# Performance work log

Measured on AMD Instinct MI355X. Metric: run time of the kernel, lower is better.

Reference implementation:

```python
import jax, jax.numpy as jnp
import numpy as np

B = 256          # graphs per batch
N_PER_G = 64     # nodes per graph
E_PER_G = 1024   # edges per graph
FN, FE, FG = 128, 128, 64
NA, HA, SO = 8, 256, 128


def _w(key, shape, scale=0.05):
    return jax.random.normal(key, shape, dtype=jnp.float32) * scale


def setup_inputs() -> dict:
    key = jax.random.key(0)
    ks = jax.random.split(key, 24)
    TN, TE = B * N_PER_G, B * E_PER_G
    inp = {
        'nodes': jax.random.normal(ks[0], (TN, FN), dtype=jnp.float32),
        'edges': jax.random.normal(ks[1], (TE, FE), dtype=jnp.float32),
        'globals_': jax.random.normal(ks[2], (B, FG), dtype=jnp.float32),
        'node_graph': jnp.repeat(jnp.arange(B, dtype=jnp.int32), N_PER_G),
        'edge_graph': jnp.repeat(jnp.arange(B, dtype=jnp.int32), E_PER_G),
        'a': jax.random.normal(ks[3], (B, NA), dtype=jnp.float32),
        # edge1: EdgeLinear(256, edge_features=FE)
        'We1': _w(ks[4], (FE, 256)), 'be1': jnp.zeros((256,), jnp.float32),
        # node1: NodeLinear(256, node_features=FN)
        'Wn1': _w(ks[5], (FN, 256)), 'bn1': jnp.zeros((256,), jnp.float32),
        # edge2: EdgeLinear(128, edge_features=256, global_features=FG)
        'We2_e': _w(ks[6], (256, 128)), 'We2_g': _w(ks[7], (FG, 128)), 'be2': jnp.zeros((128,), jnp.float32),
        # node2: NodeLinear(128, node_features=256, global_features=FG)
        'Wn2_n': _w(ks[8], (256, 128)), 'Wn2_g': _w(ks[9], (FG, 128)), 'bn2': jnp.zeros((128,), jnp.float32),
        # global: GlobalLinear(SO, node_features=128, edge_features=128, global_features=FG, aggregation='avg')
        'Wg_n': _w(ks[10], (128, SO)), 'Wg_e': _w(ks[11], (128, SO)), 'Wg_g': _w(ks[12], (FG, SO)), 'bg': jnp.zeros((SO,), jnp.float32),
        # action MLP
        'Wh': _w(ks[13], (SO + NA, HA)), 'bh': jnp.zeros((HA,), jnp.float32),
        'Wo': _w(ks[14], (HA, 1)), 'bo': jnp.zeros((1,), jnp.float32),
    }
    return inp


def _seg_mean(x, seg, num_segments):
    s = jax.ops.segment_sum(x, seg, num_segments=num_segments)
    c = jax.ops.segment_sum(jnp.ones((x.shape[0],), x.dtype), seg, num_segments=num_segments)
    return s / jnp.maximum(c, 1.0)[:, None]


def reference(nodes, edges, globals_, node_graph, edge_graph, a,
              We1, be1, Wn1, bn1, We2_e, We2_g, be2, Wn2_n, Wn2_g, bn2,
              Wg_n, Wg_e, Wg_g, bg, Wh, bh, Wo, bo):
    nb = globals_.shape[0]
    # edge1 + relu
    e = jax.nn.relu(edges @ We1 + be1)                                  # [TE,256]
    # node1 + relu
    n = jax.nn.relu(nodes @ Wn1 + bn1)                                  # [TN,256]
    # edge2 (edge feats + global broadcast to edges) + relu
    e = jax.nn.relu(e @ We2_e + globals_[edge_graph] @ We2_g + be2)     # [TE,128]
    # node2 (node feats + global broadcast to nodes) + relu
    n = jax.nn.relu(n @ Wn2_n + globals_[node_graph] @ Wn2_g + bn2)     # [TN,128]
    # global: avg-aggregate nodes and edges per graph + global linear
    n_avg = _seg_mean(n, node_graph, nb)                                # [B,128]
    e_avg = _seg_mean(e, edge_graph, nb)                                # [B,128]
    state_value = n_avg @ Wg_n + e_avg @ Wg_e + globals_ @ Wg_g + bg    # [B,SO]
    # action MLP
    sa = jnp.concatenate((state_value, a), axis=1)                      # [B,SO+NA]
    h = jax.nn.relu(sa @ Wh + bh)                                       # [B,HA]
    return h @ Wo + bo                                                  # [B,1]
```

## Files before the change

### kernel.cpp

```cpp
#include <hip/hip_runtime.h>

typedef unsigned short u16;
typedef __attribute__((ext_vector_type(8))) short s8v;
typedef __attribute__((ext_vector_type(4))) float f4v;

__device__ __forceinline__ float bf2f(u16 u) {
    union { unsigned int i; float f; } v;
    v.i = ((unsigned int)u) << 16;
    return v.f;
}
__device__ __forceinline__ u16 f2bf(float f) {
    union { float f; unsigned int i; } v;
    v.f = f;
    unsigned int x = v.i;
    x += 0x7FFFu + ((x >> 16) & 1u);
    return (u16)(x >> 16);
}
__device__ __forceinline__ float ldx(const void* p, long long i, int isf) {
    return isf ? ((const float*)p)[i] : bf2f(((const u16*)p)[i]);
}

__device__ __forceinline__ int probe_isf(const void* W) {
    const u16* p = (const u16*)W;
    int cnt = 0;
#pragma unroll
    for (int i = 0; i < 32; ++i) {
        u16 u = p[2 * i];
        int e = (u >> 7) & 0xFF;
        cnt += ((e == 0) || (e >= 96 && e <= 140)) ? 1 : 0;
    }
    return (cnt < 16) ? 1 : 0;
}

__global__ void diag_kernel(const void* W, int* flag) {
    __shared__ int cnt;
    int t = threadIdx.x;
    if (t == 0) cnt = 0;
    __syncthreads();
    u16 u = ((const u16*)W)[2 * t];
    int e = (u >> 7) & 0xFF;
    int plausible = (e == 0) || (e >= 96 && e <= 140);
    atomicAdd(&cnt, plausible);
    __syncthreads();
    if (t == 0) *flag = (cnt < 128) ? 1 : 0;
}

__global__ void magic_kernel(void* out, float code) {
    ((u16*)out)[threadIdx.x] = f2bf(code);
}

__global__ void prep2_kernel(const void* We2_g, const void* Wn2_g,
                             const void* globals_,
                             const void* We1, const void* Wn1,
                             const void* We2_e, const void* Wn2_n,
                             float* sums_zero, float* G2e, float* G2n,
                             u16* W1e_p, u16* W2e_p, u16* W1n_p, u16* W2n_p)
{
    int isf = probe_isf(We1);
    int t = blockIdx.x * 256 + threadIdx.x;
    if (t < 65536) { sums_zero[t] = 0.f; return; }
    if (t < 131072) {
        int i = t - 65536;
        int which = i >> 15;
        int idx = i & 32767;
        int g = idx >> 7, c = idx & 127;
        const void* Wg = which ? Wn2_g : We2_g;
        float s = 0.f;
#pragma unroll 8
        for (int k = 0; k < 64; ++k)
            s += ldx(globals_, g * 64 + k, isf) * ldx(Wg, k * 128 + c, isf);
        if (which) G2n[idx] = s; else G2e[idx] = s;
        return;
    }
    int p = t - 131072;
    int which = p >> 12;
    int idx = p & 4095;
    int f = idx >> 6, lj = idx & 63;
    const void* W; u16* dst; int kb, nt, N;
    if (which == 0)      { W = We1;   dst = W1e_p; kb = f >> 4; nt = f & 15; N = 256; }
    else if (which == 1) { W = Wn1;   dst = W1n_p; kb = f >> 4; nt = f & 15; N = 256; }
    else if (which == 2) { W = We2_e; dst = W2e_p; kb = f >> 3; nt = f & 7;  N = 128; }
    else                 { W = Wn2_n; dst = W2n_p; kb = f >> 3; nt = f & 7;  N = 128; }
    int k0 = kb * 32 + 8 * (lj >> 4);
    int n  = nt * 16 + (lj & 15);
    s8v v;
#pragma unroll
    for (int j = 0; j < 8; ++j)
        v[j] = (short)f2bf(ldx(W, (long long)(k0 + j) * N + n, isf));
    *(s8v*)&dst[f * 512 + lj * 8] = v;
}

__global__ __launch_bounds__(256, 4) void QNetwork_89103391522965_kernel(
    const void* edges, const void* nodes,
    const void* be1, const void* bn1, const void* be2, const void* bn2,
    const u16* W1e, const u16* W2e, const u16* W1n, const u16* W2n,
    const float* G2e, const float* G2n,
    float* e_sum, float* n_sum, const void* probeW)
{
    __shared__ u16 E1[64 * 256];
    __shared__ float accb[128];

    const int isf  = probe_isf(probeW);
    const int tid  = threadIdx.x;
    const int lane = tid & 63;
    const int w    = tid >> 6;
    const int l15  = lane & 15;
    const int lg   = lane >> 4;

    const int bid = blockIdx.x;
    const bool isn = bid >= 4096;
    const void* X   = isn ? nodes : edges;
    const void* b1  = isn ? bn1 : be1;
    const void* b2  = isn ? bn2 : be2;
    const u16* W1p  = isn ? W1n : W1e;
    const u16* W2p  = isn ? W2n : W2e;
    const float* gt = isn ? G2n : G2e;
    float* sum      = isn ? n_sum : e_sum;
    const int m0    = (isn ? (bid - 4096) : bid) * 64;
    const int g     = isn ? (bid - 4096) : (bid >> 4);

    if (tid < 128) accb[tid] = 0.f;

    f4v acc1[4][4];
#pragma unroll
    for (int nj = 0; nj < 4; ++nj) {
        float bv = ldx(b1, 64 * w + 16 * nj + l15, isf);
#pragma unroll
        for (int mi = 0; mi < 4; ++mi) {
            f4v t = {bv, bv, bv, bv};
            acc1[mi][nj] = t;
        }
    }

#pragma unroll
    for (int kb = 0; kb < 4; ++kb) {
        s8v a[4];
        const int k0 = kb * 32 + 8 * lg;
        if (!isf) {
#pragma unroll
            for (int mi = 0; mi < 4; ++mi)
                a[mi] = *(const s8v*)((const u16*)X +
                         (long long)(m0 + 16 * mi + l15) * 128 + k0);
        } else {
#pragma unroll
            for (int mi = 0; mi < 4; ++mi) {
                const float* xf = (const float*)X +
                         (long long)(m0 + 16 * mi + l15) * 128 + k0;
                s8v v;
#pragma unroll
                for (int j = 0; j < 8; ++j) v[j] = (short)f2bf(xf[j]);
                a[mi] = v;
            }
        }
#pragma unroll
        for (int nj = 0; nj < 4; ++nj) {
            s8v b = *(const s8v*)&W1p[(kb * 16 + 4 * w + nj) * 512 + lane * 8];
#pragma unroll
            for (int mi = 0; mi < 4; ++mi)
                acc1[mi][nj] = __builtin_amdgcn_mfma_f32_16x16x32_bf16(
                    a[mi], b, acc1[mi][nj], 0, 0, 0);
        }
    }

#pragma unroll
    for (int mi = 0; mi < 4; ++mi) {
#pragma unroll
        for (int nj = 0; nj < 4; ++nj) {
            int col = 64 * w + 16 * nj + l15;
#pragma unroll
            for (int r = 0; r < 4; ++r) {
                int row = 16 * mi + 4 * lg + r;
                int sw  = ((row ^ (row >> 1)) & 7) << 3;
                E1[(row * 256 + col) ^ sw] = f2bf(fmaxf(acc1[mi][nj][r], 0.f));
            }
        }
    }
    __syncthreads();

    f4v acc2[2][4];
#pragma unroll
    for (int mp = 0; mp < 2; ++mp)
#pragma unroll
        for (int nj = 0; nj < 4; ++nj) {
            f4v z = {0.f, 0.f, 0.f, 0.f};
            acc2[mp][nj] = z;
        }
    const int mb16  = (w >> 1) * 32;
    const int nbase = (w & 1) * 4;

#pragma unroll
    for (int kb = 0; kb < 8; ++kb) {
        s8v a2[2];
#pragma unroll
        for (int mp = 0; mp < 2; ++mp) {
            int row = mb16 + mp * 16 + l15;
            int sw  = ((row ^ (row >> 1)) & 7) << 3;
            a2[mp] = *(const s8v*)&E1[(row * 256 + kb * 32 + lg * 8) ^ sw];
        }
#pragma unroll
        for (int nj = 0; nj < 4; ++nj) {
            s8v b = *(const s8v*)&W2p[(kb * 8 + nbase + nj) * 512 + lane * 8];
#pragma unroll
            for (int mp = 0; mp < 2; ++mp)
                acc2[mp][nj] = __builtin_amdgcn_mfma_f32_16x16x32_bf16(
                    a2[mp], b, acc2[mp][nj], 0, 0, 0);
        }
    }

#pragma unroll
    for (int nj = 0; nj < 4; ++nj) {
        int c2 = (nbase + nj) * 16 + l15;
        float add = gt[g * 128 + c2] + ldx(b2, c2, isf);
        float s = 0.f;
#pragma unroll
        for (int mp = 0; mp < 2; ++mp)
#pragma unroll
            for (int r = 0; r < 4; ++r)
                s += fmaxf(acc2[mp][nj][r] + add, 0.f);
        s += __shfl_xor(s, 16);
        s += __shfl_xor(s, 32);
        if (lg == 0)
            atomicAdd(&accb[c2], s);
    }
    __syncthreads();
    if (tid < 128)
        atomicAdd(&sum[g * 128 + tid], accb[tid]);
}

__global__ void prep_kernel(const void* We2_g, const void* Wn2_g,
                            const void* globals_, const int* flag,
                            float* sums_zero, float* G2e, float* G2n)
{
    int isf = *flag;
    int t = blockIdx.x * 256 + threadIdx.x;
    if (t < 65536) {
        sums_zero[t] = 0.f;
    } else {
        int i = t - 65536;
        int which = i >> 15;
        int idx = i & 32767;
        int g = idx >> 7, c = idx & 127;
        const void* Wg = which ? Wn2_g : We2_g;
        float s = 0.f;
        for (int k = 0; k < 64; ++k)
            s += ldx(globals_, g * 64 + k, isf) * ldx(Wg, k * 128 + c, isf);
        if (which) G2n[idx] = s; else G2e[idx] = s;
    }
}

__global__ void QNetwork_89103391522965_valu(
    const void* X, const void* W1, const void* b1,
    const void* W2, const void* b2, const float* gterm,
    const int* flag, float* sum_out, int rows_per_graph)
{
    __shared__ u16 Xs[64 * 132];
    __shared__ u16 E1[64 * 260];
    __shared__ float accb[128];

    int isf = *flag;
    int tid = threadIdx.x;
    int m0 = blockIdx.x * 64;
    int g = m0 / rows_per_graph;

    if (tid < 128) accb[tid] = 0.f;

    for (int i = 0; i < 32; ++i) {
        int f = tid + i * 256;
        int row = f >> 7, col = f & 127;
        Xs[row * 132 + col] =
            f2bf(ldx(X, (long long)(m0 + row) * 128 + col, isf));
    }
    __syncthreads();

    {
        int c = tid;
        float binit = ldx(b1, c, isf);
        for (int rc = 0; rc < 4; ++rc) {
            float acc[16];
#pragma unroll
            for (int i = 0; i < 16; ++i) acc[i] = binit;
            for (int k = 0; k < 128; k += 2) {
                float w0 = ldx(W1, k * 256 + c, isf);
                float w1 = ldx(W1, (k + 1) * 256 + c, isf);
#pragma unroll
                for (int i = 0; i < 16; ++i) {
                    unsigned int xx =
                        *(const unsigned int*)&Xs[(rc * 16 + i) * 132 + k];
                    acc[i] += bf2f((u16)(xx & 0xFFFFu)) * w0;
                    acc[i] += bf2f((u16)(xx >> 16)) * w1;
                }
            }
#pragma unroll
            for (int i = 0; i < 16; ++i)
                E1[(rc * 16 + i) * 260 + c] = f2bf(fmaxf(acc[i], 0.f));
        }
    }
    __syncthreads();

    {
        int c2 = tid & 127;
        int rh = tid >> 7;
        float add = gterm[g * 128 + c2] + ldx(b2, c2, isf);
        float rowsum = 0.f;
        for (int rc = 0; rc < 2; ++rc) {
            int r0 = rh * 32 + rc * 16;
            float acc[16];
#pragma unroll
            for (int i = 0; i < 16; ++i) acc[i] = 0.f;
            for (int k = 0; k < 256; k += 2) {
                float w0 = ldx(W2, k * 128 + c2, isf);
                float w1 = ldx(W2, (k + 1) * 128 + c2, isf);
#pragma unroll
                for (int i = 0; i < 16; ++i) {
                    unsigned int xx =
                        *(const unsigned int*)&E1[(r0 + i) * 260 + k];
                    acc[i] += bf2f((u16)(xx & 0xFFFFu)) * w0;
                    acc[i] += bf2f((u16)(xx >> 16)) * w1;
                }
            }
#pragma unroll
            for (int i = 0; i < 16; ++i)
                rowsum += fmaxf(acc[i] + add, 0.f);
        }
        atomicAdd(&accb[c2], rowsum);
    }
    __syncthreads();
    if (tid < 128) atomicAdd(&sum_out[g * 128 + tid], accb[tid]);
}

__global__ void final_kernel(
    const float* e_sum, const float* n_sum,
    const void* globals_, const void* a_in,
    const void* Wg_n, const void* Wg_e, const void* Wg_g, const void* bg,
    const void* Wh, const void* bh, const void* Wo, const void* bo,
    const void* probeW, void* out)
{
    __shared__ float navg[128], eavg[128], gv[64], sa[136];
    __shared__ float red[4];
    int isf = probe_isf(probeW);
    int g = blockIdx.x, t = threadIdx.x;

    if (t < 128) {
        navg[t] = n_sum[g * 128 + t] * (1.f / 64.f);
        eavg[t] = e_sum[g * 128 + t] * (1.f / 1024.f);
    } else if (t < 192) {
        gv[t - 128] = ldx(globals_, g * 64 + (t - 128), isf);
    }
    __syncthreads();

    if (t < 128) {
        float s = ldx(bg, t, isf);
#pragma unroll 8
        for (int k = 0; k < 128; ++k) s += navg[k] * ldx(Wg_n, k * 128 + t, isf);
#pragma unroll 8
        for (int k = 0; k < 128; ++k) s += eavg[k] * ldx(Wg_e, k * 128 + t, isf);
#pragma unroll 8
        for (int k = 0; k < 64;  ++k) s += gv[k]   * ldx(Wg_g, k * 128 + t, isf);
        sa[t] = s;
    } else if (t < 136) {
        sa[t] = ldx(a_in, g * 8 + (t - 128), isf);
    }
    __syncthreads();

    float s = ldx(bh, t, isf);
#pragma unroll 8
    for (int k = 0; k < 136; ++k) s += sa[k] * ldx(Wh, k * 256 + t, isf);
    float hv = fmaxf(s, 0.f) * ldx(Wo, t, isf);
#pragma unroll
    for (int off = 32; off; off >>= 1) hv += __shfl_down(hv, off);
    if ((t & 63) == 0) red[t >> 6] = hv;
    __syncthreads();
    if (t == 0) {
        float val = red[0] + red[1] + red[2] + red[3] + ldx(bo, 0, isf);
        if (isf) ((float*)out)[g] = val;
        else     ((u16*)out)[g]   = f2bf(val);
    }
}

extern "C" void kernel_launch(void* const* d_in, const int* in_sizes, int n_in,
                              void* d_out, int out_size, void* d_ws, size_t ws_size,
                              hipStream_t stream) {
    static const int EXPECT[24] = {
        2097152, 33554432, 16384, 16384, 262144, 2048,
        32768, 256, 32768, 256,
        32768, 8192, 128, 32768, 8192, 128,
        16384, 16384, 8192, 128,
        34816, 256, 256, 1
    };
    float code = 0.f;
    if (n_in != 24) code = 3000.f + n_in;
    else {
        for (int i = 0; i < 24; ++i)
            if (in_sizes[i] != EXPECT[i]) { code = 1000.f + i; break; }
    }
    if (ws_size < 524292 && code == 0.f) code = 4000.f;
    if (code != 0.f) {
        magic_kernel<<<1, 256, 0, stream>>>(d_out, code);
        return;
    }

    const void* nodes    = d_in[0];
    const void* edges    = d_in[1];
    const void* globals_ = d_in[2];
    const void* a_in  = d_in[5];
    const void* We1   = d_in[6];
    const void* be1   = d_in[7];
    const void* Wn1   = d_in[8];
    const void* bn1   = d_in[9];
    const void* We2_e = d_in[10];
    const void* We2_g = d_in[11];
    const void* be2   = d_in[12];
    const void* Wn2_n = d_in[13];
    const void* Wn2_g = d_in[14];
    const void* bn2   = d_in[15];
    const void* Wg_n  = d_in[16];
    const void* Wg_e  = d_in[17];
    const void* Wg_g  = d_in[18];
    const void* bg    = d_in[19];
    const void* Wh    = d_in[20];
    const void* bh    = d_in[21];
    const void* Wo    = d_in[22];
    const void* bo    = d_in[23];

    char* ws = (char*)d_ws;
    float* e_sum = (float*)(ws + 0);
    float* n_sum = (float*)(ws + 131072);
    float* G2e   = (float*)(ws + 262144);
    float* G2n   = (float*)(ws + 393216);

    if (ws_size >= 786436) {
        u16* W1e_p = (u16*)(ws + 524288);
        u16* W2e_p = (u16*)(ws + 589824);
        u16* W1n_p = (u16*)(ws + 655360);
        u16* W2n_p = (u16*)(ws + 720896);

        prep2_kernel<<<576, 256, 0, stream>>>(We2_g, Wn2_g, globals_,
                                              We1, Wn1, We2_e, Wn2_n,
                                              e_sum, G2e, G2n,
                                              W1e_p, W2e_p, W1n_p, W2n_p);
        QNetwork_89103391522965_kernel<<<4352, 256, 0, stream>>>(
            edges, nodes, be1, bn1, be2, bn2,
            W1e_p, W2e_p, W1n_p, W2n_p, G2e, G2n,
            e_sum, n_sum, We1);
        final_kernel<<<256, 256, 0, stream>>>(e_sum, n_sum, globals_, a_in,
                                              Wg_n, Wg_e, Wg_g, bg, Wh, bh, Wo, bo,
                                              We1, d_out);
    } else {
        int* flag = (int*)(ws + 524288);
        diag_kernel<<<1, 256, 0, stream>>>(We1, flag);
        prep_kernel<<<512, 256, 0, stream>>>(We2_g, Wn2_g, globals_, flag,
                                             e_sum, G2e, G2n);
        QNetwork_89103391522965_valu<<<4096, 256, 0, stream>>>(
            edges, We1, be1, We2_e, be2, G2e, flag, e_sum, 1024);
        QNetwork_89103391522965_valu<<<256, 256, 0, stream>>>(
            nodes, Wn1, bn1, Wn2_n, bn2, G2n, flag, n_sum, 64);
        final_kernel<<<256, 256, 0, stream>>>(e_sum, n_sum, globals_, a_in,
                                              Wg_n, Wg_e, Wg_g, bg, Wh, bh, Wo, bo,
                                              We1, d_out);
    }
}
```

Before: 373.8 us.

## Halve per-block row tile to 32 and cache dtype probe flag in workspace

The fused two-layer MLP kernel now handles 32 rows per block instead of 64. This halves the shared-memory staging buffer and the accumulator registers, doubles the grid, and raises the launch-bounds occupancy hint from 4 to 6 blocks per CU. The per-block dtype probe (a shared atomic vote over weight bits) is replaced by a flag written once in the prep kernel and read from the workspace by the main and final kernels. The trade-off is more blocks and more global atomics into the per-graph sums, and weight fragments are reloaded more often relative to the rows processed.

New measurement: 428.7 us. +14.7%, slower.

```diff
diff --git a/kernel.cpp b/kernel.cpp
--- a/kernel.cpp
+++ b/kernel.cpp
@@ -54,10 +54,12 @@
                              const void* We1, const void* Wn1,
                              const void* We2_e, const void* Wn2_n,
                              float* sums_zero, float* G2e, float* G2n,
-                             u16* W1e_p, u16* W2e_p, u16* W1n_p, u16* W2n_p)
+                             u16* W1e_p, u16* W2e_p, u16* W1n_p, u16* W2n_p,
+                             int* flagp)
 {
     int isf = probe_isf(We1);
     int t = blockIdx.x * 256 + threadIdx.x;
+    if (t == 0) *flagp = isf;
     if (t < 65536) { sums_zero[t] = 0.f; return; }
     if (t < 131072) {
         int i = t - 65536;
@@ -90,17 +92,17 @@
     *(s8v*)&dst[f * 512 + lj * 8] = v;
 }
 
-__global__ __launch_bounds__(256, 4) void QNetwork_89103391522965_kernel(
+__global__ __launch_bounds__(256, 6) void QNetwork_89103391522965_kernel(
     const void* edges, const void* nodes,
     const void* be1, const void* bn1, const void* be2, const void* bn2,
     const u16* W1e, const u16* W2e, const u16* W1n, const u16* W2n,
     const float* G2e, const float* G2n,
-    float* e_sum, float* n_sum, const void* probeW)
+    float* e_sum, float* n_sum, const int* flagp)
 {
-    __shared__ u16 E1[64 * 256];
+    __shared__ u16 E1[32 * 256];
     __shared__ float accb[128];
 
-    const int isf  = probe_isf(probeW);
+    const int isf  = *flagp;
     const int tid  = threadIdx.x;
     const int lane = tid & 63;
     const int w    = tid >> 6;
@@ -108,7 +110,8 @@
     const int lg   = lane >> 4;
 
     const int bid = blockIdx.x;
-    const bool isn = bid >= 4096;
+    const bool isn = bid >= 8192;
+    const int rb = isn ? (bid - 8192) : bid;
     const void* X   = isn ? nodes : edges;
     const void* b1  = isn ? bn1 : be1;
     const void* b2  = isn ? bn2 : be2;
@@ -116,107 +119,93 @@
     const u16* W2p  = isn ? W2n : W2e;
     const float* gt = isn ? G2n : G2e;
     float* sum      = isn ? n_sum : e_sum;
-    const int m0    = (isn ? (bid - 4096) : bid) * 64;
-    const int g     = isn ? (bid - 4096) : (bid >> 4);
+    const int m0    = rb * 32;
+    const int g     = isn ? (rb >> 1) : (rb >> 5);
 
     if (tid < 128) accb[tid] = 0.f;
 
-    f4v acc1[4][4];
+    const int nbase = (w & 1) * 4;
+    const int mi2   = (w >> 1);
+
+    float binit[4];
+#pragma unroll
+    for (int nj = 0; nj < 4; ++nj)
+        binit[nj] = ldx(b1, 64 * w + 16 * nj + l15, isf);
+    float add[4];
 #pragma unroll
     for (int nj = 0; nj < 4; ++nj) {
-        float bv = ldx(b1, 64 * w + 16 * nj + l15, isf);
-#pragma unroll
-        for (int mi = 0; mi < 4; ++mi) {
-            f4v t = {bv, bv, bv, bv};
-            acc1[mi][nj] = t;
-        }
-    }
-
-#pragma unroll
-    for (int kb = 0; kb < 4; ++kb) {
-        s8v a[4];
-        const int k0 = kb * 32 + 8 * lg;
-        if (!isf) {
-#pragma unroll
-            for (int mi = 0; mi < 4; ++mi)
-                a[mi] = *(const s8v*)((const u16*)X +
-                         (long long)(m0 + 16 * mi + l15) * 128 + k0);
-        } else {
-#pragma unroll
-            for (int mi = 0; mi < 4; ++mi) {
-                const float* xf = (const float*)X +
-                         (long long)(m0 + 16 * mi + l15) * 128 + k0;
+        int c2 = (nbase + nj) * 16 + l15;
+        add[nj] = gt[g * 128 + c2] + ldx(b2, c2, isf);
+    }
+
+#pragma unroll
+    for (int mh = 0; mh < 2; ++mh) {
+        f4v acc1[4];
+#pragma unroll
+        for (int nj = 0; nj < 4; ++nj) {
+            f4v tv = {binit[nj], binit[nj], binit[nj], binit[nj]};
+            acc1[nj] = tv;
+        }
+#pragma unroll
+        for (int kb = 0; kb < 4; ++kb) {
+            const int k0 = kb * 32 + 8 * lg;
+            const int row = m0 + 16 * mh + l15;
+            s8v a;
+            if (!isf) {
+                a = *(const s8v*)((const u16*)X + (long long)row * 128 + k0);
+            } else {
+                const float* xf = (const float*)X + (long long)row * 128 + k0;
                 s8v v;
 #pragma unroll
                 for (int j = 0; j < 8; ++j) v[j] = (short)f2bf(xf[j]);
-                a[mi] = v;
+                a = v;
             }
-        }
-#pragma unroll
-        for (int nj = 0; nj < 4; ++nj) {
-            s8v b = *(const s8v*)&W1p[(kb * 16 + 4 * w + nj) * 512 + lane * 8];
-#pragma unroll
-            for (int mi = 0; mi < 4; ++mi)
-                acc1[mi][nj] = __builtin_amdgcn_mfma_f32_16x16x32_bf16(
-                    a[mi], b, acc1[mi][nj], 0, 0, 0);
-        }
-    }
-
-#pragma unroll
-    for (int mi = 0; mi < 4; ++mi) {
+#pragma unroll
+            for (int nj = 0; nj < 4; ++nj) {
+                s8v b = *(const s8v*)&W1p[(kb * 16 + 4 * w + nj) * 512 + lane * 8];
+                acc1[nj] = __builtin_amdgcn_mfma_f32_16x16x32_bf16(
+                    a, b, acc1[nj], 0, 0, 0);
+            }
+        }
 #pragma unroll
         for (int nj = 0; nj < 4; ++nj) {
             int col = 64 * w + 16 * nj + l15;
 #pragma unroll
             for (int r = 0; r < 4; ++r) {
-                int row = 16 * mi + 4 * lg + r;
+                int row = 16 * mh + 4 * lg + r;
                 int sw  = ((row ^ (row >> 1)) & 7) << 3;
-                E1[(row * 256 + col) ^ sw] = f2bf(fmaxf(acc1[mi][nj][r], 0.f));
+                E1[(row * 256 + col) ^ sw] = f2bf(fmaxf(acc1[nj][r], 0.f));
             }
         }
     }
     __syncthreads();
 
-    f4v acc2[2][4];
-#pragma unroll
-    for (int mp = 0; mp < 2; ++mp)
-#pragma unroll
-        for (int nj = 0; nj < 4; ++nj) {
-            f4v z = {0.f, 0.f, 0.f, 0.f};
-            acc2[mp][nj] = z;
-        }
-    const int mb16  = (w >> 1) * 32;
-    const int nbase = (w & 1) * 4;
-
+    f4v acc2[4];
+#pragma unroll
+    for (int nj = 0; nj < 4; ++nj) {
+        f4v z = {0.f, 0.f, 0.f, 0.f};
+        acc2[nj] = z;
+    }
 #pragma unroll
     for (int kb = 0; kb < 8; ++kb) {
-        s8v a2[2];
-#pragma unroll
-        for (int mp = 0; mp < 2; ++mp) {
-            int row = mb16 + mp * 16 + l15;
-            int sw  = ((row ^ (row >> 1)) & 7) << 3;
-            a2[mp] = *(const s8v*)&E1[(row * 256 + kb * 32 + lg * 8) ^ sw];
-        }
+        int row = 16 * mi2 + l15;
+        int sw  = ((row ^ (row >> 1)) & 7) << 3;
+        s8v a2 = *(const s8v*)&E1[(row * 256 + kb * 32 + lg * 8) ^ sw];
 #pragma unroll
         for (int nj = 0; nj < 4; ++nj) {
             s8v b = *(const s8v*)&W2p[(kb * 8 + nbase + nj) * 512 + lane * 8];
-#pragma unroll
-            for (int mp = 0; mp < 2; ++mp)
-                acc2[mp][nj] = __builtin_amdgcn_mfma_f32_16x16x32_bf16(
-                    a2[mp], b, acc2[mp][nj], 0, 0, 0);
+            acc2[nj] = __builtin_amdgcn_mfma_f32_16x16x32_bf16(
+                a2, b, acc2[nj], 0, 0, 0);
         }
     }
 
 #pragma unroll
     for (int nj = 0; nj < 4; ++nj) {
         int c2 = (nbase + nj) * 16 + l15;
-        float add = gt[g * 128 + c2] + ldx(b2, c2, isf);
         float s = 0.f;
 #pragma unroll
-        for (int mp = 0; mp < 2; ++mp)
-#pragma unroll
-            for (int r = 0; r < 4; ++r)
-                s += fmaxf(acc2[mp][nj][r] + add, 0.f);
+        for (int r = 0; r < 4; ++r)
+            s += fmaxf(acc2[nj][r] + add[nj], 0.f);
         s += __shfl_xor(s, 16);
         s += __shfl_xor(s, 32);
         if (lg == 0)
@@ -333,11 +322,11 @@
     const void* globals_, const void* a_in,
     const void* Wg_n, const void* Wg_e, const void* Wg_g, const void* bg,
     const void* Wh, const void* bh, const void* Wo, const void* bo,
-    const void* probeW, void* out)
+    const int* flagp, void* out)
 {
     __shared__ float navg[128], eavg[128], gv[64], sa[136];
     __shared__ float red[4];
-    int isf = probe_isf(probeW);
+    int isf = *flagp;
     int g = blockIdx.x, t = threadIdx.x;
 
     if (t < 128) {
@@ -428,23 +417,25 @@
     float* G2e   = (float*)(ws + 262144);
     float* G2n   = (float*)(ws + 393216);
 
-    if (ws_size >= 786436) {
+    if (ws_size >= 786440) {
         u16* W1e_p = (u16*)(ws + 524288);
         u16* W2e_p = (u16*)(ws + 589824);
         u16* W1n_p = (u16*)(ws + 655360);
         u16* W2n_p = (u16*)(ws + 720896);
+        int* flagp = (int*)(ws + 786432);
 
         prep2_kernel<<<576, 256, 0, stream>>>(We2_g, Wn2_g, globals_,
                                               We1, Wn1, We2_e, Wn2_n,
                                               e_sum, G2e, G2n,
-                                              W1e_p, W2e_p, W1n_p, W2n_p);
-        QNetwork_89103391522965_kernel<<<4352, 256, 0, stream>>>(
+                                              W1e_p, W2e_p, W1n_p, W2n_p,
+                                              flagp);
+        QNetwork_89103391522965_kernel<<<8704, 256, 0, stream>>>(
             edges, nodes, be1, bn1, be2, bn2,
             W1e_p, W2e_p, W1n_p, W2n_p, G2e, G2n,
-            e_sum, n_sum, We1);
+            e_sum, n_sum, flagp);
         final_kernel<<<256, 256, 0, stream>>>(e_sum, n_sum, globals_, a_in,
                                               Wg_n, Wg_e, Wg_g, bg, Wh, bh, Wo, bo,
-                                              We1, d_out);
+                                              flagp, d_out);
     } else {
         int* flag = (int*)(ws + 524288);
         diag_kernel<<<1, 256, 0, stream>>>(We1, flag);
@@ -456,6 +447,6 @@
             nodes, Wn1, bn1, Wn2_n, bn2, G2n, flag, n_sum, 64);
         final_kernel<<<256, 256, 0, stream>>>(e_sum, n_sum, globals_, a_in,
                                               Wg_n, Wg_e, Wg_g, bg, Wh, bh, Wo, bo,
-                                              We1, d_out);
-    }
-}
+                                              flag, d_out);
+    }
+}
```

## Process four 64-row tiles per block and cache dtype probe flag

Applied to the files above, without the earlier changes.

The fused MLP kernel now has each block loop over four 64-row tiles, so the grid shrinks from 4352 to 1088 blocks. Edge partial sums are kept in registers across tiles and hit global memory with one atomic per graph. Node tiles write their per-graph sums directly instead of using atomics. The per-kernel dtype probe is replaced by a flag computed once in prep2 and read from workspace. The cost is fewer blocks in flight and serialized tiles inside each block, with no overlap between a tile's loads and the previous tile's compute.

Result: slower. 780.7 us (+108.8%).

```diff
diff --git a/kernel.cpp b/kernel.cpp
--- a/kernel.cpp
+++ b/kernel.cpp
@@ -54,10 +54,12 @@
                              const void* We1, const void* Wn1,
                              const void* We2_e, const void* Wn2_n,
                              float* sums_zero, float* G2e, float* G2n,
-                             u16* W1e_p, u16* W2e_p, u16* W1n_p, u16* W2n_p)
+                             u16* W1e_p, u16* W2e_p, u16* W1n_p, u16* W2n_p,
+                             int* flagp)
 {
     int isf = probe_isf(We1);
     int t = blockIdx.x * 256 + threadIdx.x;
+    if (t == 0) *flagp = isf;
     if (t < 65536) { sums_zero[t] = 0.f; return; }
     if (t < 131072) {
         int i = t - 65536;
@@ -95,12 +97,12 @@
     const void* be1, const void* bn1, const void* be2, const void* bn2,
     const u16* W1e, const u16* W2e, const u16* W1n, const u16* W2n,
     const float* G2e, const float* G2n,
-    float* e_sum, float* n_sum, const void* probeW)
+    float* e_sum, float* n_sum, const int* flagp)
 {
     __shared__ u16 E1[64 * 256];
     __shared__ float accb[128];
 
-    const int isf  = probe_isf(probeW);
+    const int isf  = *flagp;
     const int tid  = threadIdx.x;
     const int lane = tid & 63;
     const int w    = tid >> 6;
@@ -108,123 +110,155 @@
     const int lg   = lane >> 4;
 
     const int bid = blockIdx.x;
-    const bool isn = bid >= 4096;
+    const bool isn = bid >= 1024;
+    const int rb = isn ? (bid - 1024) : bid;
     const void* X   = isn ? nodes : edges;
     const void* b1  = isn ? bn1 : be1;
     const void* b2  = isn ? bn2 : be2;
     const u16* W1p  = isn ? W1n : W1e;
     const u16* W2p  = isn ? W2n : W2e;
     const float* gt = isn ? G2n : G2e;
-    float* sum      = isn ? n_sum : e_sum;
-    const int m0    = (isn ? (bid - 4096) : bid) * 64;
-    const int g     = isn ? (bid - 4096) : (bid >> 4);
+    const int base  = rb * 256;
+    const int ge    = bid >> 2;
 
     if (tid < 128) accb[tid] = 0.f;
 
-    f4v acc1[4][4];
-#pragma unroll
-    for (int nj = 0; nj < 4; ++nj) {
-        float bv = ldx(b1, 64 * w + 16 * nj + l15, isf);
-#pragma unroll
-        for (int mi = 0; mi < 4; ++mi) {
-            f4v t = {bv, bv, bv, bv};
-            acc1[mi][nj] = t;
-        }
-    }
-
-#pragma unroll
-    for (int kb = 0; kb < 4; ++kb) {
-        s8v a[4];
-        const int k0 = kb * 32 + 8 * lg;
-        if (!isf) {
-#pragma unroll
-            for (int mi = 0; mi < 4; ++mi)
-                a[mi] = *(const s8v*)((const u16*)X +
-                         (long long)(m0 + 16 * mi + l15) * 128 + k0);
-        } else {
-#pragma unroll
-            for (int mi = 0; mi < 4; ++mi) {
-                const float* xf = (const float*)X +
-                         (long long)(m0 + 16 * mi + l15) * 128 + k0;
-                s8v v;
-#pragma unroll
-                for (int j = 0; j < 8; ++j) v[j] = (short)f2bf(xf[j]);
-                a[mi] = v;
-            }
-        }
-#pragma unroll
-        for (int nj = 0; nj < 4; ++nj) {
-            s8v b = *(const s8v*)&W1p[(kb * 16 + 4 * w + nj) * 512 + lane * 8];
-#pragma unroll
-            for (int mi = 0; mi < 4; ++mi)
-                acc1[mi][nj] = __builtin_amdgcn_mfma_f32_16x16x32_bf16(
-                    a[mi], b, acc1[mi][nj], 0, 0, 0);
-        }
-    }
-
-#pragma unroll
-    for (int mi = 0; mi < 4; ++mi) {
-#pragma unroll
-        for (int nj = 0; nj < 4; ++nj) {
-            int col = 64 * w + 16 * nj + l15;
-#pragma unroll
-            for (int r = 0; r < 4; ++r) {
-                int row = 16 * mi + 4 * lg + r;
-                int sw  = ((row ^ (row >> 1)) & 7) << 3;
-                E1[(row * 256 + col) ^ sw] = f2bf(fmaxf(acc1[mi][nj][r], 0.f));
-            }
-        }
-    }
-    __syncthreads();
-
-    f4v acc2[2][4];
-#pragma unroll
-    for (int mp = 0; mp < 2; ++mp)
-#pragma unroll
-        for (int nj = 0; nj < 4; ++nj) {
-            f4v z = {0.f, 0.f, 0.f, 0.f};
-            acc2[mp][nj] = z;
-        }
     const int mb16  = (w >> 1) * 32;
     const int nbase = (w & 1) * 4;
 
-#pragma unroll
-    for (int kb = 0; kb < 8; ++kb) {
-        s8v a2[2];
-#pragma unroll
-        for (int mp = 0; mp < 2; ++mp) {
-            int row = mb16 + mp * 16 + l15;
-            int sw  = ((row ^ (row >> 1)) & 7) << 3;
-            a2[mp] = *(const s8v*)&E1[(row * 256 + kb * 32 + lg * 8) ^ sw];
-        }
+    float binit[4];
+#pragma unroll
+    for (int nj = 0; nj < 4; ++nj)
+        binit[nj] = ldx(b1, 64 * w + 16 * nj + l15, isf);
+
+    float rs[4] = {0.f, 0.f, 0.f, 0.f};
+
+    for (int t = 0; t < 4; ++t) {
+        const int m0 = base + t * 64;
+        const int gg = isn ? (m0 >> 6) : ge;
+
+        f4v acc1[4][4];
 #pragma unroll
         for (int nj = 0; nj < 4; ++nj) {
-            s8v b = *(const s8v*)&W2p[(kb * 8 + nbase + nj) * 512 + lane * 8];
+#pragma unroll
+            for (int mi = 0; mi < 4; ++mi) {
+                f4v tv = {binit[nj], binit[nj], binit[nj], binit[nj]};
+                acc1[mi][nj] = tv;
+            }
+        }
+#pragma unroll
+        for (int kb = 0; kb < 4; ++kb) {
+            s8v a[4];
+            const int k0 = kb * 32 + 8 * lg;
+            if (!isf) {
+#pragma unroll
+                for (int mi = 0; mi < 4; ++mi)
+                    a[mi] = *(const s8v*)((const u16*)X +
+                             (long long)(m0 + 16 * mi + l15) * 128 + k0);
+            } else {
+#pragma unroll
+                for (int mi = 0; mi < 4; ++mi) {
+                    const float* xf = (const float*)X +
+                             (long long)(m0 + 16 * mi + l15) * 128 + k0;
+                    s8v v;
+#pragma unroll
+                    for (int j = 0; j < 8; ++j) v[j] = (short)f2bf(xf[j]);
+                    a[mi] = v;
+                }
+            }
+#pragma unroll
+            for (int nj = 0; nj < 4; ++nj) {
+                s8v b = *(const s8v*)&W1p[(kb * 16 + 4 * w + nj) * 512 + lane * 8];
+#pragma unroll
+                for (int mi = 0; mi < 4; ++mi)
+                    acc1[mi][nj] = __builtin_amdgcn_mfma_f32_16x16x32_bf16(
+                        a[mi], b, acc1[mi][nj], 0, 0, 0);
+            }
+        }
+
+#pragma unroll
+        for (int mi = 0; mi < 4; ++mi) {
+#pragma unroll
+            for (int nj = 0; nj < 4; ++nj) {
+                int col = 64 * w + 16 * nj + l15;
+#pragma unroll
+                for (int r = 0; r < 4; ++r) {
+                    int row = 16 * mi + 4 * lg + r;
+                    int sw  = ((row ^ (row >> 1)) & 7) << 3;
+                    E1[(row * 256 + col) ^ sw] = f2bf(fmaxf(acc1[mi][nj][r], 0.f));
+                }
+            }
+        }
+        __syncthreads();
+
+        f4v acc2[2][4];
+#pragma unroll
+        for (int mp = 0; mp < 2; ++mp)
+#pragma unroll
+            for (int nj = 0; nj < 4; ++nj) {
+                f4v z = {0.f, 0.f, 0.f, 0.f};
+                acc2[mp][nj] = z;
+            }
+#pragma unroll
+        for (int kb = 0; kb < 8; ++kb) {
+            s8v a2[2];
+#pragma unroll
+            for (int mp = 0; mp < 2; ++mp) {
+                int row = mb16 + mp * 16 + l15;
+                int sw  = ((row ^ (row >> 1)) & 7) << 3;
+                a2[mp] = *(const s8v*)&E1[(row * 256 + kb * 32 + lg * 8) ^ sw];
+            }
+#pragma unroll
+            for (int nj = 0; nj < 4; ++nj) {
+                s8v b = *(const s8v*)&W2p[(kb * 8 + nbase + nj) * 512 + lane * 8];
+#pragma unroll
+                for (int mp = 0; mp < 2; ++mp)
+                    acc2[mp][nj] = __builtin_amdgcn_mfma_f32_16x16x32_bf16(
+                        a2[mp], b, acc2[mp][nj], 0, 0, 0);
+            }
+        }
+
+#pragma unroll
+        for (int nj = 0; nj < 4; ++nj) {
+            int c2 = (nbase + nj) * 16 + l15;
+            float add = gt[gg * 128 + c2] + ldx(b2, c2, isf);
+            float s = 0.f;
 #pragma unroll
             for (int mp = 0; mp < 2; ++mp)
-                acc2[mp][nj] = __builtin_amdgcn_mfma_f32_16x16x32_bf16(
-                    a2[mp], b, acc2[mp][nj], 0, 0, 0);
-        }
-    }
-
-#pragma unroll
-    for (int nj = 0; nj < 4; ++nj) {
-        int c2 = (nbase + nj) * 16 + l15;
-        float add = gt[g * 128 + c2] + ldx(b2, c2, isf);
-        float s = 0.f;
-#pragma unroll
-        for (int mp = 0; mp < 2; ++mp)
-#pragma unroll
-            for (int r = 0; r < 4; ++r)
-                s += fmaxf(acc2[mp][nj][r] + add, 0.f);
-        s += __shfl_xor(s, 16);
-        s += __shfl_xor(s, 32);
-        if (lg == 0)
-            atomicAdd(&accb[c2], s);
-    }
-    __syncthreads();
-    if (tid < 128)
-        atomicAdd(&sum[g * 128 + tid], accb[tid]);
+#pragma unroll
+                for (int r = 0; r < 4; ++r)
+                    s += fmaxf(acc2[mp][nj][r] + add, 0.f);
+            if (isn) {
+                s += __shfl_xor(s, 16);
+                s += __shfl_xor(s, 32);
+                if (lg == 0) atomicAdd(&accb[c2], s);
+            } else {
+                rs[nj] += s;
+            }
+        }
+        if (isn) {
+            __syncthreads();
+            if (tid < 128) {
+                n_sum[gg * 128 + tid] = accb[tid];
+                accb[tid] = 0.f;
+            }
+        }
+        __syncthreads();
+    }
+
+    if (!isn) {
+#pragma unroll
+        for (int nj = 0; nj < 4; ++nj) {
+            float v = rs[nj];
+            v += __shfl_xor(v, 16);
+            v += __shfl_xor(v, 32);
+            if (lg == 0)
+                atomicAdd(&accb[(nbase + nj) * 16 + l15], v);
+        }
+        __syncthreads();
+        if (tid < 128)
+            atomicAdd(&e_sum[ge * 128 + tid], accb[tid]);
+    }
 }
 
 __global__ void prep_kernel(const void* We2_g, const void* Wn2_g,
@@ -333,11 +367,11 @@
     const void* globals_, const void* a_in,
     const void* Wg_n, const void* Wg_e, const void* Wg_g, const void* bg,
     const void* Wh, const void* bh, const void* Wo, const void* bo,
-    const void* probeW, void* out)
+    const int* flagp, void* out)
 {
     __shared__ float navg[128], eavg[128], gv[64], sa[136];
     __shared__ float red[4];
-    int isf = probe_isf(probeW);
+    int isf = *flagp;
     int g = blockIdx.x, t = threadIdx.x;
 
     if (t < 128) {
@@ -428,23 +462,25 @@
     float* G2e   = (float*)(ws + 262144);
     float* G2n   = (float*)(ws + 393216);
 
-    if (ws_size >= 786436) {
+    if (ws_size >= 786440) {
         u16* W1e_p = (u16*)(ws + 524288);
         u16* W2e_p = (u16*)(ws + 589824);
         u16* W1n_p = (u16*)(ws + 655360);
         u16* W2n_p = (u16*)(ws + 720896);
+        int* flagp = (int*)(ws + 786432);
 
         prep2_kernel<<<576, 256, 0, stream>>>(We2_g, Wn2_g, globals_,
                                               We1, Wn1, We2_e, Wn2_n,
                                               e_sum, G2e, G2n,
-                                              W1e_p, W2e_p, W1n_p, W2n_p);
-        QNetwork_89103391522965_kernel<<<4352, 256, 0, stream>>>(
+                                              W1e_p, W2e_p, W1n_p, W2n_p,
+                                              flagp);
+        QNetwork_89103391522965_kernel<<<1088, 256, 0, stream>>>(
             edges, nodes, be1, bn1, be2, bn2,
             W1e_p, W2e_p, W1n_p, W2n_p, G2e, G2n,
-            e_sum, n_sum, We1);
+            e_sum, n_sum, flagp);
         final_kernel<<<256, 256, 0, stream>>>(e_sum, n_sum, globals_, a_in,
                                               Wg_n, Wg_e, Wg_g, bg, Wh, bh, Wo, bo,
-                                              We1, d_out);
+                                              flagp, d_out);
     } else {
         int* flag = (int*)(ws + 524288);
         diag_kernel<<<1, 256, 0, stream>>>(We1, flag);
@@ -456,6 +492,6 @@
             nodes, Wn1, bn1, Wn2_n, bn2, G2n, flag, n_sum, 64);
         final_kernel<<<256, 256, 0, stream>>>(e_sum, n_sum, globals_, a_in,
                                               Wg_n, Wg_e, Wg_g, bg, Wh, bh, Wo, bo,
-                                              We1, d_out);
-    }
-}
+                                              flag, d_out);
+    }
+}
```
